# Performance work log

Hardware: AMD Instinct MI355X
Metric: run time of the kernel (lower is better)

Reference implementation:

```python
import jax, jax.numpy as jnp
import numpy as np

B, N, D, H = 8, 1024, 768, 12
HD = D // H


def setup_inputs() -> dict:
    key = jax.random.key(0)
    ks = jax.random.split(key, 9)
    s = 1.0 / np.sqrt(D)
    return {
        "x": jax.random.normal(ks[0], (B, N, D), dtype=jnp.float32),
        "Wq": jax.random.normal(ks[1], (D, D), dtype=jnp.float32) * s,
        "bq": jax.random.normal(ks[2], (D,), dtype=jnp.float32) * 0.01,
        "Wk": jax.random.normal(ks[3], (D, D), dtype=jnp.float32) * s,
        "bk": jax.random.normal(ks[4], (D,), dtype=jnp.float32) * 0.01,
        "Wv": jax.random.normal(ks[5], (D, D), dtype=jnp.float32) * s,
        "bv": jax.random.normal(ks[6], (D,), dtype=jnp.float32) * 0.01,
        "Wo": jax.random.normal(ks[7], (D, D), dtype=jnp.float32) * s,
        "bo": jax.random.normal(ks[8], (D,), dtype=jnp.float32) * 0.01,
    }


def reference(x, Wq, bq, Wk, bk, Wv, bv, Wo, bo):
    b, n, d = x.shape
    split = lambda t: t.reshape(b, n, H, HD).transpose(0, 2, 1, 3)  # b h n d
    q = split(x @ Wq + bq)
    k = split(x @ Wk + bk)
    v = split(x @ Wv + bv)
    energy = jnp.einsum('bhqd,bhkd->bhqk', q, k)
    # NOTE: module scales AFTER softmax by sqrt(emb_size) (not head_dim) -- faithful.
    att = jax.nn.softmax(energy, axis=-1) / jnp.sqrt(jnp.float32(D)).astype(x.dtype)
    out = jnp.einsum('bhqk,bhkd->bhqd', att, v)
    out = out.transpose(0, 2, 1, 3).reshape(b, n, d)
    return out @ Wo + bo
```

## Files before the change

kernel.cpp:

```cpp
#include <hip/hip_runtime.h>

#define B_  8
#define N_  1024
#define D_  768
#define H_  12
#define HD_ 64
#define M_  (B_ * N_)
#define WELEM (D_ * D_)
#define XELEM ((size_t)M_ * D_)

typedef _Float16 f16;
typedef f16   f16x8  __attribute__((ext_vector_type(8)));
typedef short bf16x8 __attribute__((ext_vector_type(8)));
typedef float f32x4  __attribute__((ext_vector_type(4)));
typedef unsigned short u16;

__device__ __forceinline__ u16 f2bf(float f) {
    unsigned int x = __float_as_uint(f);
    return (u16)((x + 0x7fffu + ((x >> 16) & 1u)) >> 16);
}
__device__ __forceinline__ float bf2f(u16 u) {
    return __uint_as_float(((unsigned int)u) << 16);
}
__device__ __forceinline__ u16 f2h(float f) {
    return __builtin_bit_cast(u16, (f16)f);
}
__device__ __forceinline__ unsigned int cvtpk_bf16(float lo, float hi) {
    unsigned int r;
    asm("v_cvt_pk_bf16_f32 %0, %1, %2" : "=v"(r) : "v"(lo), "v"(hi));
    return r;
}
#if __has_builtin(__builtin_amdgcn_exp2f)
#define EXP2F(x) __builtin_amdgcn_exp2f(x)
#else
#define EXP2F(x) exp2f(x)
#endif

#define LOG2E_   1.4426950408889634f
#define EXPBIAS_ 28.853900817779268f

typedef __attribute__((address_space(3))) unsigned int       as3_u32;
typedef __attribute__((address_space(1))) const unsigned int as1_u32;
__device__ __forceinline__ void dma16(const void* g, void* l) {
    __builtin_amdgcn_global_load_lds((as1_u32*)g, (as3_u32*)l, 16, 0, 0);
}

__global__ __launch_bounds__(256) void cvt_x(const float* __restrict__ X,
                                             u16* __restrict__ Xh) {
    int idx = blockIdx.x * 256 + threadIdx.x;
    float4 v = ((const float4*)X)[idx];
    ushort4 o = {f2h(v.x), f2h(v.y), f2h(v.z), f2h(v.w)};
    ((ushort4*)Xh)[idx] = o;
}

__global__ __launch_bounds__(256) void cvt_w(
    const float* __restrict__ w0, const float* __restrict__ w1,
    const float* __restrict__ w2, const float* __restrict__ w3,
    u16* __restrict__ Wt) {
    const float* W = blockIdx.y == 0 ? w0 : blockIdx.y == 1 ? w1
                   : blockIdx.y == 2 ? w2 : w3;
    u16* dst = Wt + (size_t)blockIdx.y * WELEM;
    const int t  = threadIdx.x;
    const int tk = (blockIdx.x % 12) * 64, tn = (blockIdx.x / 12) * 64;
    __shared__ __align__(16) float tile[64][68];
#pragma unroll
    for (int i = 0; i < 4; ++i) {
        int r = (t >> 4) + i * 16, c4 = (t & 15) * 4;
        float4 v = *(const float4*)(W + (size_t)(tk + r) * D_ + tn + c4);
        *(float4*)&tile[r][c4] = v;
    }
    __syncthreads();
#pragma unroll
    for (int i = 0; i < 4; ++i) {
        int nr = (t >> 4) + i * 16, kc = (t & 15) * 4;
        ushort4 o = {f2h(tile[kc + 0][nr]), f2h(tile[kc + 1][nr]),
                     f2h(tile[kc + 2][nr]), f2h(tile[kc + 3][nr])};
        *(ushort4*)(dst + (size_t)(tn + nr) * D_ + tk + kc) = o;
    }
}

__global__ __launch_bounds__(256) void gemm_qkv(
    const u16* __restrict__ Xh, const u16* __restrict__ Wt,
    const float* __restrict__ bq, const float* __restrict__ bk,
    const float* __restrict__ bv, u16* __restrict__ Qf,
    u16* __restrict__ Kf, u16* __restrict__ Vt) {
    __shared__ __align__(16) u16 As[128 * 64];
    __shared__ __align__(16) u16 Bs[64 * 64];

    const int id  = blockIdx.x;
    const int xcd = id & 7, idx = id >> 3;
    const int m0  = (xcd * 8 + idx / 36) * 128;
    const int rem = idx % 36;
    const int z   = rem / 12, n0 = (rem % 12) * 64;

    const u16* Wz = Wt + (size_t)z * WELEM;
    const float* bias = z == 0 ? bq : z == 1 ? bk : bv;

    const int t = threadIdx.x, lane = t & 63, w = t >> 6;
    const int wm = w >> 1, wn = w & 1;
    const int quad = lane >> 4, ln = lane & 15;
    const int drow = lane >> 3, dcl = (lane & 7) ^ ((lane >> 3) & 7);

    f32x4 acc[4][2] = {};
    for (int k0 = 0; k0 < D_; k0 += 64) {
        __syncthreads();
#pragma unroll
        for (int j = 0; j < 4; ++j) {
            int i = w * 4 + j, row = i * 8 + drow;
            dma16(Xh + (size_t)(m0 + row) * D_ + k0 + dcl * 8, &As[i * 512]);
        }
#pragma unroll
        for (int j = 0; j < 2; ++j) {
            int i = w * 2 + j, row = i * 8 + drow;
            dma16(Wz + (size_t)(n0 + row) * D_ + k0 + dcl * 8, &Bs[i * 512]);
        }
        __syncthreads();
        f16x8 a[4][2], b[2][2];
#pragma unroll
        for (int mt = 0; mt < 4; ++mt)
#pragma unroll
            for (int ks = 0; ks < 2; ++ks)
                a[mt][ks] = *(const f16x8*)&As[(wm * 64 + mt * 16 + ln) * 64 +
                                               (((ks * 4 + quad) ^ (ln & 7)) * 8)];
#pragma unroll
        for (int nt = 0; nt < 2; ++nt)
#pragma unroll
            for (int ks = 0; ks < 2; ++ks)
                b[nt][ks] = *(const f16x8*)&Bs[(wn * 32 + nt * 16 + ln) * 64 +
                                               (((ks * 4 + quad) ^ (ln & 7)) * 8)];
#pragma unroll
        for (int mt = 0; mt < 4; ++mt)
#pragma unroll
            for (int nt = 0; nt < 2; ++nt) {
                acc[mt][nt] = __builtin_amdgcn_mfma_f32_16x16x32_f16(
                    a[mt][0], b[nt][0], acc[mt][nt], 0, 0, 0);
                acc[mt][nt] = __builtin_amdgcn_mfma_f32_16x16x32_f16(
                    a[mt][1], b[nt][1], acc[mt][nt], 0, 0, 0);
            }
    }
    const int h = n0 >> 6;
#pragma unroll
    for (int nt = 0; nt < 2; ++nt) {
        int hd = wn * 32 + nt * 16 + ln;
        float bv_ = bias[n0 + hd];
#pragma unroll
        for (int mt = 0; mt < 4; ++mt) {
            int mb = m0 + wm * 64 + mt * 16 + quad * 4;
            int bb = mb >> 10, ns = mb & 1023;
            if (z == 0) {
#pragma unroll
                for (int r = 0; r < 4; ++r)
                    Qf[(((size_t)bb * H_ + h) * N_ + ns + r) * HD_ + hd] =
                        f2h((acc[mt][nt][r] + bv_) * LOG2E_);
            } else if (z == 1) {
#pragma unroll
                for (int r = 0; r < 4; ++r)
                    Kf[(((size_t)bb * H_ + h) * N_ + ns + r) * HD_ + hd] =
                        f2h(acc[mt][nt][r] + bv_);
            } else {
                ushort4 o = {f2bf(acc[mt][nt][0] + bv_), f2bf(acc[mt][nt][1] + bv_),
                             f2bf(acc[mt][nt][2] + bv_), f2bf(acc[mt][nt][3] + bv_)};
                *(ushort4*)(Vt + (((size_t)bb * H_ + h) * HD_ + hd) * N_ + ns) = o;
            }
        }
    }
}

__global__ __launch_bounds__(256) void attn_mfma(
    const u16* __restrict__ Qg, const u16* __restrict__ Kg,
    const u16* __restrict__ Vtg, u16* __restrict__ Og) {
    __shared__ __align__(16) u16 Ks[2][64 * 64];
    __shared__ __align__(16) u16 Vs[2][64 * 64];
    __shared__ __align__(16) u16 Ps[128 * 72];

    const int t = threadIdx.x, lane = t & 63, w = t >> 6;
    const int quad = lane >> 4, ln = lane & 15;
    const int drow = lane >> 3, dcl = (lane & 7) ^ ((lane >> 3) & 7);
    const int id  = blockIdx.x;
    const int id2 = (id & 7) * 96 + (id >> 3);
    const int bh  = id2 >> 3, qt = id2 & 7;
    const u16* Qh  = Qg  + ((size_t)bh * N_ + qt * 128) * HD_;
    const u16* Kh  = Kg  + (size_t)bh * N_ * HD_;
    const u16* Vth = Vtg + (size_t)bh * HD_ * N_;
    u16*       Oh  = Og  + ((size_t)bh * N_ + qt * 128) * HD_;

    const int rho0 = (w * 2 + 0) * 8 + drow;
    const int rho1 = (w * 2 + 1) * 8 + drow;
    const int gk0  = 4 * (rho0 & 15) + (rho0 >> 4);
    const int gk1  = 4 * (rho1 & 15) + (rho1 >> 4);

    f16x8 aq[2][2];
#pragma unroll
    for (int mt = 0; mt < 2; ++mt)
#pragma unroll
        for (int ks = 0; ks < 2; ++ks)
            aq[mt][ks] = *(const f16x8*)(Qh + (size_t)(w * 32 + mt * 16 + ln) * HD_ +
                                         ks * 32 + quad * 8);

    float lsum[2][4] = {};
    f32x4 oacc[2][4] = {};

    dma16(Kh + (size_t)(0 * 64 + gk0) * HD_ + dcl * 8, &Ks[0][(w * 2 + 0) * 512]);
    dma16(Kh + (size_t)(0 * 64 + gk1) * HD_ + dcl * 8, &Ks[0][(w * 2 + 1) * 512]);
    dma16(Vth + (size_t)rho0 * N_ + 0 * 64 + dcl * 8, &Vs[0][(w * 2 + 0) * 512]);
    dma16(Vth + (size_t)rho1 * N_ + 0 * 64 + dcl * 8, &Vs[0][(w * 2 + 1) * 512]);

#pragma unroll 2
    for (int kt = 0; kt < 16; ++kt) {
        const int cur = kt & 1;
        if (kt < 15) {
            const int nk = (kt + 1) * 64;
            dma16(Kh + (size_t)(nk + gk0) * HD_ + dcl * 8, &Ks[cur ^ 1][(w * 2 + 0) * 512]);
            dma16(Kh + (size_t)(nk + gk1) * HD_ + dcl * 8, &Ks[cur ^ 1][(w * 2 + 1) * 512]);
            dma16(Vth + (size_t)rho0 * N_ + nk + dcl * 8, &Vs[cur ^ 1][(w * 2 + 0) * 512]);
            dma16(Vth + (size_t)rho1 * N_ + nk + dcl * 8, &Vs[cur ^ 1][(w * 2 + 1) * 512]);
            asm volatile("s_waitcnt vmcnt(4)" ::: "memory");
        } else {
            asm volatile("s_waitcnt vmcnt(0)" ::: "memory");
        }
        __builtin_amdgcn_s_barrier();
        __builtin_amdgcn_sched_barrier(0);

        f32x4 sf[2][4];
        __builtin_amdgcn_s_setprio(1);
#pragma unroll
        for (int nt = 0; nt < 4; ++nt) {
            f16x8 b0 = *(const f16x8*)&Ks[cur][(nt * 16 + ln) * 64 + ((quad) ^ (ln & 7)) * 8];
            f16x8 b1 = *(const f16x8*)&Ks[cur][(nt * 16 + ln) * 64 + ((4 + quad) ^ (ln & 7)) * 8];
#pragma unroll
            for (int mt = 0; mt < 2; ++mt) {
                f32x4 zz = {};
                sf[mt][nt] = __builtin_amdgcn_mfma_f32_16x16x32_f16(aq[mt][0], b0, zz, 0, 0, 0);
                sf[mt][nt] = __builtin_amdgcn_mfma_f32_16x16x32_f16(aq[mt][1], b1, sf[mt][nt], 0, 0, 0);
            }
        }
        __builtin_amdgcn_s_setprio(0);

#pragma unroll
        for (int mt = 0; mt < 2; ++mt)
#pragma unroll
            for (int r = 0; r < 4; ++r) {
                float e0 = EXP2F(sf[mt][0][r] - EXPBIAS_);
                float e1 = EXP2F(sf[mt][1][r] - EXPBIAS_);
                float e2 = EXP2F(sf[mt][2][r] - EXPBIAS_);
                float e3 = EXP2F(sf[mt][3][r] - EXPBIAS_);
                uint2 pk;
                pk.x = cvtpk_bf16(e0, e1);
                pk.y = cvtpk_bf16(e2, e3);
                int q = w * 32 + mt * 16 + quad * 4 + r;
                *(uint2*)&Ps[q * 72 + ln * 4] = pk;
                lsum[mt][r] += __uint_as_float(pk.x << 16) +
                               __uint_as_float(pk.x & 0xffff0000u) +
                               __uint_as_float(pk.y << 16) +
                               __uint_as_float(pk.y & 0xffff0000u);
            }

        __builtin_amdgcn_s_setprio(1);
#pragma unroll
        for (int mt = 0; mt < 2; ++mt) {
            bf16x8 ap0 = *(const bf16x8*)&Ps[(w * 32 + mt * 16 + ln) * 72 + quad * 8];
            bf16x8 ap1 = *(const bf16x8*)&Ps[(w * 32 + mt * 16 + ln) * 72 + 32 + quad * 8];
#pragma unroll
            for (int nt = 0; nt < 4; ++nt) {
                bf16x8 bv0 = *(const bf16x8*)&Vs[cur][(nt * 16 + ln) * 64 +
                                                      ((quad ^ (ln & 7)) * 8)];
                oacc[mt][nt] = __builtin_amdgcn_mfma_f32_16x16x32_bf16(
                    ap0, bv0, oacc[mt][nt], 0, 0, 0);
                bf16x8 bv1 = *(const bf16x8*)&Vs[cur][(nt * 16 + ln) * 64 +
                                                      (((4 + quad) ^ (ln & 7)) * 8)];
                oacc[mt][nt] = __builtin_amdgcn_mfma_f32_16x16x32_bf16(
                    ap1, bv1, oacc[mt][nt], 0, 0, 0);
            }
        }
        __builtin_amdgcn_s_setprio(0);
        __builtin_amdgcn_sched_barrier(0);
        __builtin_amdgcn_s_barrier();
    }

    const float sc = 0.036084391824351615f;
#pragma unroll
    for (int mt = 0; mt < 2; ++mt)
#pragma unroll
        for (int r = 0; r < 4; ++r) {
            float l = lsum[mt][r];
            l += __shfl_xor(l, 1);
            l += __shfl_xor(l, 2);
            l += __shfl_xor(l, 4);
            l += __shfl_xor(l, 8);
            float inv = sc / l;
#pragma unroll
            for (int nt = 0; nt < 4; ++nt)
                Oh[(size_t)(w * 32 + mt * 16 + quad * 4 + r) * HD_ + nt * 16 + ln] =
                    f2h(oacc[mt][nt][r] * inv);
        }
}

__global__ __launch_bounds__(256) void gemm_out(
    const u16* __restrict__ Ob, const u16* __restrict__ Wto,
    const float* __restrict__ bias, float* __restrict__ Out) {
    __shared__ __align__(16) u16 As[128 * 64];
    __shared__ __align__(16) u16 Bs[64 * 64];

    const int id  = blockIdx.x;
    const int id2 = (id & 7) * 96 + (id >> 3);
    const int m0  = (id2 / 12) * 128, n0 = (id2 % 12) * 64;

    const int t = threadIdx.x, lane = t & 63, w = t >> 6;
    const int wm = w >> 1, wn = w & 1;
    const int quad = lane >> 4, ln = lane & 15;
    const int drow = lane >> 3, dcl = (lane & 7) ^ ((lane >> 3) & 7);

    f32x4 acc[4][2] = {};
    for (int k0 = 0; k0 < D_; k0 += 64) {
        int head = k0 >> 6;
        __syncthreads();
#pragma unroll
        for (int j = 0; j < 4; ++j) {
            int i = w * 4 + j, row = i * 8 + drow;
            int m = m0 + row, bb = m >> 10, ns = m & 1023;
            dma16(Ob + (((size_t)bb * H_ + head) * N_ + ns) * HD_ + dcl * 8, &As[i * 512]);
        }
#pragma unroll
        for (int j = 0; j < 2; ++j) {
            int i = w * 2 + j, row = i * 8 + drow;
            dma16(Wto + (size_t)(n0 + row) * D_ + k0 + dcl * 8, &Bs[i * 512]);
        }
        __syncthreads();
        f16x8 a[4][2], b[2][2];
#pragma unroll
        for (int mt = 0; mt < 4; ++mt)
#pragma unroll
            for (int ks = 0; ks < 2; ++ks)
                a[mt][ks] = *(const f16x8*)&As[(wm * 64 + mt * 16 + ln) * 64 +
                                               (((ks * 4 + quad) ^ (ln & 7)) * 8)];
#pragma unroll
        for (int nt = 0; nt < 2; ++nt)
#pragma unroll
            for (int ks = 0; ks < 2; ++ks)
                b[nt][ks] = *(const f16x8*)&Bs[(wn * 32 + nt * 16 + ln) * 64 +
                                               (((ks * 4 + quad) ^ (ln & 7)) * 8)];
#pragma unroll
        for (int mt = 0; mt < 4; ++mt)
#pragma unroll
            for (int nt = 0; nt < 2; ++nt) {
                acc[mt][nt] = __builtin_amdgcn_mfma_f32_16x16x32_f16(
                    a[mt][0], b[nt][0], acc[mt][nt], 0, 0, 0);
                acc[mt][nt] = __builtin_amdgcn_mfma_f32_16x16x32_f16(
                    a[mt][1], b[nt][1], acc[mt][nt], 0, 0, 0);
            }
    }
#pragma unroll
    for (int nt = 0; nt < 2; ++nt) {
        int n = n0 + wn * 32 + nt * 16 + ln;
        float bv_ = bias[n];
#pragma unroll
        for (int mt = 0; mt < 4; ++mt) {
            int mb = m0 + wm * 64 + mt * 16 + quad * 4;
#pragma unroll
            for (int r = 0; r < 4; ++r)
                Out[(size_t)(mb + r) * D_ + n] = acc[mt][nt][r] + bv_;
        }
    }
}

extern "C" void kernel_launch(void* const* d_in, const int* in_sizes, int n_in,
                              void* d_out, int out_size, void* d_ws, size_t ws_size,
                              hipStream_t stream) {
    const float* x  = (const float*)d_in[0];
    const float* Wq = (const float*)d_in[1];
    const float* bq = (const float*)d_in[2];
    const float* Wk = (const float*)d_in[3];
    const float* bk = (const float*)d_in[4];
    const float* Wv = (const float*)d_in[5];
    const float* bv = (const float*)d_in[6];
    const float* Wo = (const float*)d_in[7];
    const float* bo = (const float*)d_in[8];

    u16* Xh = (u16*)d_ws;
    u16* Wt = Xh + XELEM;
    u16* Qf = Wt + 4 * (size_t)WELEM;
    u16* Kf = Qf + XELEM;
    u16* Vt = Kf + XELEM;
    u16* Ob = Vt + XELEM;

    cvt_x<<<dim3((int)(XELEM / 4 / 256)), 256, 0, stream>>>(x, Xh);
    cvt_w<<<dim3(144, 4), 256, 0, stream>>>(Wq, Wk, Wv, Wo, Wt);
    gemm_qkv<<<dim3(2304), 256, 0, stream>>>(Xh, Wt, bq, bk, bv, Qf, Kf, Vt);
    attn_mfma<<<dim3(768), 256, 0, stream>>>(Qf, Kf, Vt, Ob);
    gemm_out<<<dim3(768), 256, 0, stream>>>(
        Ob, Wt + 3 * (size_t)WELEM, bo, (float*)d_out);
}
```

Baseline: 201.9 us.

## Widen QKV GEMM tiles, compute softmax row sums via MFMA, restructure attention barriers

The QKV projection GEMM moves from 128x64 to 128x128 output tiles, so each block loads more of B per A tile and the grid is halved. In attention, the exp bias is folded into the QK MFMA accumulator init, and the per-row softmax sums now come from an extra MFMA against a ones vector instead of scalar adds and cross-lane shuffles. The loop now uses one barrier per iteration and waits for all outstanding loads before issuing the next prefetch. This cuts prefetch overlap in exchange for fewer syncs, and the larger tile raises register pressure.

Result: slower. 209.4 us (+3.7%).

```diff
diff --git a/kernel.cpp b/kernel.cpp
--- a/kernel.cpp
+++ b/kernel.cpp
@@ -18,9 +18,6 @@
 __device__ __forceinline__ u16 f2bf(float f) {
     unsigned int x = __float_as_uint(f);
     return (u16)((x + 0x7fffu + ((x >> 16) & 1u)) >> 16);
-}
-__device__ __forceinline__ float bf2f(u16 u) {
-    return __uint_as_float(((unsigned int)u) << 16);
 }
 __device__ __forceinline__ u16 f2h(float f) {
     return __builtin_bit_cast(u16, (f16)f);
@@ -85,13 +82,13 @@
     const float* __restrict__ bv, u16* __restrict__ Qf,
     u16* __restrict__ Kf, u16* __restrict__ Vt) {
     __shared__ __align__(16) u16 As[128 * 64];
-    __shared__ __align__(16) u16 Bs[64 * 64];
+    __shared__ __align__(16) u16 Bs[128 * 64];
 
     const int id  = blockIdx.x;
     const int xcd = id & 7, idx = id >> 3;
-    const int m0  = (xcd * 8 + idx / 36) * 128;
-    const int rem = idx % 36;
-    const int z   = rem / 12, n0 = (rem % 12) * 64;
+    const int m0  = (xcd * 8 + idx / 18) * 128;
+    const int rem = idx % 18;
+    const int z   = rem / 6, n0 = (rem % 6) * 128;
 
     const u16* Wz = Wt + (size_t)z * WELEM;
     const float* bias = z == 0 ? bq : z == 1 ? bk : bv;
@@ -101,7 +98,7 @@
     const int quad = lane >> 4, ln = lane & 15;
     const int drow = lane >> 3, dcl = (lane & 7) ^ ((lane >> 3) & 7);
 
-    f32x4 acc[4][2] = {};
+    f32x4 acc[4][4] = {};
     for (int k0 = 0; k0 < D_; k0 += 64) {
         __syncthreads();
 #pragma unroll
@@ -110,12 +107,12 @@
             dma16(Xh + (size_t)(m0 + row) * D_ + k0 + dcl * 8, &As[i * 512]);
         }
 #pragma unroll
-        for (int j = 0; j < 2; ++j) {
-            int i = w * 2 + j, row = i * 8 + drow;
+        for (int j = 0; j < 4; ++j) {
+            int i = w * 4 + j, row = i * 8 + drow;
             dma16(Wz + (size_t)(n0 + row) * D_ + k0 + dcl * 8, &Bs[i * 512]);
         }
         __syncthreads();
-        f16x8 a[4][2], b[2][2];
+        f16x8 a[4][2], b[4][2];
 #pragma unroll
         for (int mt = 0; mt < 4; ++mt)
 #pragma unroll
@@ -123,26 +120,26 @@
                 a[mt][ks] = *(const f16x8*)&As[(wm * 64 + mt * 16 + ln) * 64 +
                                                (((ks * 4 + quad) ^ (ln & 7)) * 8)];
 #pragma unroll
-        for (int nt = 0; nt < 2; ++nt)
+        for (int nt = 0; nt < 4; ++nt)
 #pragma unroll
             for (int ks = 0; ks < 2; ++ks)
-                b[nt][ks] = *(const f16x8*)&Bs[(wn * 32 + nt * 16 + ln) * 64 +
+                b[nt][ks] = *(const f16x8*)&Bs[(wn * 64 + nt * 16 + ln) * 64 +
                                                (((ks * 4 + quad) ^ (ln & 7)) * 8)];
 #pragma unroll
         for (int mt = 0; mt < 4; ++mt)
 #pragma unroll
-            for (int nt = 0; nt < 2; ++nt) {
+            for (int nt = 0; nt < 4; ++nt) {
                 acc[mt][nt] = __builtin_amdgcn_mfma_f32_16x16x32_f16(
                     a[mt][0], b[nt][0], acc[mt][nt], 0, 0, 0);
                 acc[mt][nt] = __builtin_amdgcn_mfma_f32_16x16x32_f16(
                     a[mt][1], b[nt][1], acc[mt][nt], 0, 0, 0);
             }
     }
-    const int h = n0 >> 6;
-#pragma unroll
-    for (int nt = 0; nt < 2; ++nt) {
-        int hd = wn * 32 + nt * 16 + ln;
-        float bv_ = bias[n0 + hd];
+    const int h = (n0 >> 6) + wn;
+#pragma unroll
+    for (int nt = 0; nt < 4; ++nt) {
+        int hd = nt * 16 + ln;
+        float bv_ = bias[n0 + wn * 64 + hd];
 #pragma unroll
         for (int mt = 0; mt < 4; ++mt) {
             int mb = m0 + wm * 64 + mt * 16 + quad * 4;
@@ -197,29 +194,31 @@
             aq[mt][ks] = *(const f16x8*)(Qh + (size_t)(w * 32 + mt * 16 + ln) * HD_ +
                                          ks * 32 + quad * 8);
 
-    float lsum[2][4] = {};
+    const bf16x8 pone = {0x3F80, 0x3F80, 0x3F80, 0x3F80,
+                         0x3F80, 0x3F80, 0x3F80, 0x3F80};
+    const f32x4 nb = {-EXPBIAS_, -EXPBIAS_, -EXPBIAS_, -EXPBIAS_};
+
     f32x4 oacc[2][4] = {};
-
-    dma16(Kh + (size_t)(0 * 64 + gk0) * HD_ + dcl * 8, &Ks[0][(w * 2 + 0) * 512]);
-    dma16(Kh + (size_t)(0 * 64 + gk1) * HD_ + dcl * 8, &Ks[0][(w * 2 + 1) * 512]);
-    dma16(Vth + (size_t)rho0 * N_ + 0 * 64 + dcl * 8, &Vs[0][(w * 2 + 0) * 512]);
-    dma16(Vth + (size_t)rho1 * N_ + 0 * 64 + dcl * 8, &Vs[0][(w * 2 + 1) * 512]);
+    f32x4 lacc[2] = {};
+
+    dma16(Kh + (size_t)gk0 * HD_ + dcl * 8, &Ks[0][(w * 2 + 0) * 512]);
+    dma16(Kh + (size_t)gk1 * HD_ + dcl * 8, &Ks[0][(w * 2 + 1) * 512]);
+    dma16(Vth + (size_t)rho0 * N_ + dcl * 8, &Vs[0][(w * 2 + 0) * 512]);
+    dma16(Vth + (size_t)rho1 * N_ + dcl * 8, &Vs[0][(w * 2 + 1) * 512]);
 
 #pragma unroll 2
     for (int kt = 0; kt < 16; ++kt) {
         const int cur = kt & 1;
+        asm volatile("s_waitcnt vmcnt(0)" ::: "memory");
+        __builtin_amdgcn_s_barrier();
+        __builtin_amdgcn_sched_barrier(0);
         if (kt < 15) {
             const int nk = (kt + 1) * 64;
             dma16(Kh + (size_t)(nk + gk0) * HD_ + dcl * 8, &Ks[cur ^ 1][(w * 2 + 0) * 512]);
             dma16(Kh + (size_t)(nk + gk1) * HD_ + dcl * 8, &Ks[cur ^ 1][(w * 2 + 1) * 512]);
             dma16(Vth + (size_t)rho0 * N_ + nk + dcl * 8, &Vs[cur ^ 1][(w * 2 + 0) * 512]);
             dma16(Vth + (size_t)rho1 * N_ + nk + dcl * 8, &Vs[cur ^ 1][(w * 2 + 1) * 512]);
-            asm volatile("s_waitcnt vmcnt(4)" ::: "memory");
-        } else {
-            asm volatile("s_waitcnt vmcnt(0)" ::: "memory");
-        }
-        __builtin_amdgcn_s_barrier();
-        __builtin_amdgcn_sched_barrier(0);
+        }
 
         f32x4 sf[2][4];
         __builtin_amdgcn_s_setprio(1);
@@ -229,8 +228,7 @@
             f16x8 b1 = *(const f16x8*)&Ks[cur][(nt * 16 + ln) * 64 + ((4 + quad) ^ (ln & 7)) * 8];
 #pragma unroll
             for (int mt = 0; mt < 2; ++mt) {
-                f32x4 zz = {};
-                sf[mt][nt] = __builtin_amdgcn_mfma_f32_16x16x32_f16(aq[mt][0], b0, zz, 0, 0, 0);
+                sf[mt][nt] = __builtin_amdgcn_mfma_f32_16x16x32_f16(aq[mt][0], b0, nb, 0, 0, 0);
                 sf[mt][nt] = __builtin_amdgcn_mfma_f32_16x16x32_f16(aq[mt][1], b1, sf[mt][nt], 0, 0, 0);
             }
         }
@@ -240,19 +238,15 @@
         for (int mt = 0; mt < 2; ++mt)
 #pragma unroll
             for (int r = 0; r < 4; ++r) {
-                float e0 = EXP2F(sf[mt][0][r] - EXPBIAS_);
-                float e1 = EXP2F(sf[mt][1][r] - EXPBIAS_);
-                float e2 = EXP2F(sf[mt][2][r] - EXPBIAS_);
-                float e3 = EXP2F(sf[mt][3][r] - EXPBIAS_);
+                float e0 = EXP2F(sf[mt][0][r]);
+                float e1 = EXP2F(sf[mt][1][r]);
+                float e2 = EXP2F(sf[mt][2][r]);
+                float e3 = EXP2F(sf[mt][3][r]);
                 uint2 pk;
                 pk.x = cvtpk_bf16(e0, e1);
                 pk.y = cvtpk_bf16(e2, e3);
                 int q = w * 32 + mt * 16 + quad * 4 + r;
                 *(uint2*)&Ps[q * 72 + ln * 4] = pk;
-                lsum[mt][r] += __uint_as_float(pk.x << 16) +
-                               __uint_as_float(pk.x & 0xffff0000u) +
-                               __uint_as_float(pk.y << 16) +
-                               __uint_as_float(pk.y & 0xffff0000u);
             }
 
         __builtin_amdgcn_s_setprio(1);
@@ -260,6 +254,8 @@
         for (int mt = 0; mt < 2; ++mt) {
             bf16x8 ap0 = *(const bf16x8*)&Ps[(w * 32 + mt * 16 + ln) * 72 + quad * 8];
             bf16x8 ap1 = *(const bf16x8*)&Ps[(w * 32 + mt * 16 + ln) * 72 + 32 + quad * 8];
+            lacc[mt] = __builtin_amdgcn_mfma_f32_16x16x32_bf16(ap0, pone, lacc[mt], 0, 0, 0);
+            lacc[mt] = __builtin_amdgcn_mfma_f32_16x16x32_bf16(ap1, pone, lacc[mt], 0, 0, 0);
 #pragma unroll
             for (int nt = 0; nt < 4; ++nt) {
                 bf16x8 bv0 = *(const bf16x8*)&Vs[cur][(nt * 16 + ln) * 64 +
@@ -273,8 +269,6 @@
             }
         }
         __builtin_amdgcn_s_setprio(0);
-        __builtin_amdgcn_sched_barrier(0);
-        __builtin_amdgcn_s_barrier();
     }
 
     const float sc = 0.036084391824351615f;
@@ -282,12 +276,7 @@
     for (int mt = 0; mt < 2; ++mt)
 #pragma unroll
         for (int r = 0; r < 4; ++r) {
-            float l = lsum[mt][r];
-            l += __shfl_xor(l, 1);
-            l += __shfl_xor(l, 2);
-            l += __shfl_xor(l, 4);
-            l += __shfl_xor(l, 8);
-            float inv = sc / l;
+            float inv = sc / lacc[mt][r];
 #pragma unroll
             for (int nt = 0; nt < 4; ++nt)
                 Oh[(size_t)(w * 32 + mt * 16 + quad * 4 + r) * HD_ + nt * 16 + ln] =
@@ -385,7 +374,7 @@
 
     cvt_x<<<dim3((int)(XELEM / 4 / 256)), 256, 0, stream>>>(x, Xh);
     cvt_w<<<dim3(144, 4), 256, 0, stream>>>(Wq, Wk, Wv, Wo, Wt);
-    gemm_qkv<<<dim3(2304), 256, 0, stream>>>(Xh, Wt, bq, bk, bv, Qf, Kf, Vt);
+    gemm_qkv<<<dim3(1152), 256, 0, stream>>>(Xh, Wt, bq, bk, bv, Qf, Kf, Vt);
     attn_mfma<<<dim3(768), 256, 0, stream>>>(Qf, Kf, Vt, Ob);
     gemm_out<<<dim3(768), 256, 0, stream>>>(
         Ob, Wt + 3 * (size_t)WELEM, bo, (float*)d_out);
```
